# Optimization experiments

Measured on AMD Instinct MI355X. Metric: run time of the kernel, lower is better.

Reference implementation:

```python
import jax, jax.numpy as jnp
import numpy as np

A, D, H, NACT = 8, 128, 64, 16  # n_agents, input_shape, rnn_hidden_dim, n_actions
B = 16384


def setup_inputs() -> dict:
    key = jax.random.key(0)
    ks = jax.random.split(key, 12)
    s = 1.0 / np.sqrt(H)
    si = 1.0 / np.sqrt(D)
    inp = {
        'inputs': jax.random.normal(ks[0], (B * A, D), dtype=jnp.float32),
        'hidden_state': jax.random.normal(ks[1], (B, A, H), dtype=jnp.float32),
        # stacked per-agent (non-shared) weights, PyTorch default-init scale
        'W1': jax.random.uniform(ks[2], (A, H, D), jnp.float32, -si, si),
        'b1': jax.random.uniform(ks[3], (A, H), jnp.float32, -si, si),
        'W_ih': jax.random.uniform(ks[4], (A, 3 * H, H), jnp.float32, -s, s),
        'b_ih': jax.random.uniform(ks[5], (A, 3 * H), jnp.float32, -s, s),
        'W_hh': jax.random.uniform(ks[6], (A, 3 * H, H), jnp.float32, -s, s),
        'b_hh': jax.random.uniform(ks[7], (A, 3 * H), jnp.float32, -s, s),
        'W2': jax.random.uniform(ks[8], (A, NACT, H), jnp.float32, -s, s),
        'b2': jax.random.uniform(ks[9], (A, NACT), jnp.float32, -s, s),
    }
    return inp


def reference(inputs, hidden_state, W1, b1, W_ih, b_ih, W_hh, b_hh, W2, b2):
    x = inputs.reshape(-1, A, D)                 # [B, A, D]
    h = hidden_state.reshape(-1, A, H)           # [B, A, H]
    # fc1 + ReLU, batched over agents
    z1 = jax.nn.relu(jnp.einsum('bad,ahd->bah', x, W1) + b1)
    # GRUCell (PyTorch convention: gates r, z, n)
    gi = jnp.einsum('bah,agh->bag', z1, W_ih) + b_ih   # [B, A, 3H]
    gh = jnp.einsum('bah,agh->bag', h, W_hh) + b_hh
    i_r, i_z, i_n = jnp.split(gi, 3, axis=-1)
    h_r, h_z, h_n = jnp.split(gh, 3, axis=-1)
    r = jax.nn.sigmoid(i_r + h_r)
    z = jax.nn.sigmoid(i_z + h_z)
    n = jnp.tanh(i_n + r * h_n)
    h_new = (1.0 - z) * n + z * h                # [B, A, H]
    # fc2
    q = jnp.einsum('bah,anh->ban', h_new, W2) + b2   # [B, A, NACT]
    # match torch: cat(qs, dim=-1).view(-1, n_actions) == reshape [B*A, NACT]
    return q.reshape(-1, NACT), h_new
```

## Files before the change

kernel.cpp:

```cpp
#include <hip/hip_runtime.h>
#include <hip/hip_bf16.h>
#include <cstddef>

#define NAGENT 8
#define DIN    128
#define HID    64
#define NACT   16

typedef __attribute__((ext_vector_type(8))) short bf16x8;
typedef __attribute__((ext_vector_type(4))) float f32x4;

__device__ __forceinline__ short f2bf(float f) {
    __hip_bfloat16 h = __float2bfloat16(f);
    union { __hip_bfloat16 h; short s; } u; u.h = h;
    return u.s;
}
__device__ __forceinline__ float sigmoid_f(float v) { return 1.0f / (1.0f + __expf(-v)); }
__device__ __forceinline__ float tanh_f(float v) {
    v = fminf(fmaxf(v, -15.0f), 15.0f);
    float e = __expf(2.0f * v);
    return (e - 1.0f) / (e + 1.0f);
}
__device__ __forceinline__ bf16x8 cvt8pair(float4 v0, float4 v1) {
    bf16x8 r;
    r[0] = f2bf(v0.x); r[1] = f2bf(v0.y); r[2] = f2bf(v0.z); r[3] = f2bf(v0.w);
    r[4] = f2bf(v1.x); r[5] = f2bf(v1.y); r[6] = f2bf(v1.z); r[7] = f2bf(v1.w);
    return r;
}
__device__ __forceinline__ void gload_lds16(const void* g, void* l) {
    __builtin_amdgcn_global_load_lds(
        (const __attribute__((address_space(1))) unsigned int*)g,
        (__attribute__((address_space(3))) unsigned int*)l, 16, 0, 0);
}

extern "C" __global__ void __launch_bounds__(256)
conv_weights_packed(const float* __restrict__ W1, const float* __restrict__ Wih,
                    const float* __restrict__ Whh, const float* __restrict__ W2,
                    short* __restrict__ ws)
{
    const int a = blockIdx.y;
    const int c = blockIdx.x * 256 + threadIdx.x;
    if (c >= 4224) return;
    const int lane = c & 63, lr = lane & 15, lk = lane >> 4;
    const float* src;
    if (c < 1024) {
        int n = c >> 8, k = (c >> 6) & 3;
        src = W1 + a * 8192 + (n * 16 + lr) * 128 + k * 32 + lk * 8;
    } else if (c < 2560) {
        int idx = (c - 1024) >> 6;
        int g = idx >> 3, n = (idx >> 1) & 3, kk = idx & 1;
        src = Wih + a * 12288 + (g * 64 + n * 16 + lr) * 64 + kk * 32 + lk * 8;
    } else if (c < 4096) {
        int idx = (c - 2560) >> 6;
        int g = idx >> 3, n = (idx >> 1) & 3, kk = idx & 1;
        src = Whh + a * 12288 + (g * 64 + n * 16 + lr) * 64 + kk * 32 + lk * 8;
    } else {
        int kk = (c - 4096) >> 6;
        src = W2 + a * 1024 + lr * 64 + kk * 32 + lk * 8;
    }
    float4 v0 = ((const float4*)src)[0];
    float4 v1 = ((const float4*)src)[1];
    bf16x8 o = cvt8pair(v0, v1);
    *(bf16x8*)(ws + (size_t)a * 33792 + (size_t)c * 8) = o;
}

extern "C" __global__ void __launch_bounds__(256, 4)
rnn_main(const float* __restrict__ x,
         const float* __restrict__ hin,
         const float* __restrict__ b1, const float* __restrict__ bih,
         const float* __restrict__ bhh, const float* __restrict__ b2,
         const short* __restrict__ wsp,
         float* __restrict__ qout,
         float* __restrict__ hout)
{
    const int bid  = blockIdx.x;
    const int a    = bid & 7;
    const int t    = threadIdx.x;
    const int wid  = t >> 6;
    const int lane = t & 63;
    const int lr   = lane & 15;
    const int lk   = lane >> 4;

    __shared__ short wbuf[2 * 3072];
    __shared__ short zs[4 * 1024];
    char* zb = (char*)(zs + wid * 1024);
    const char* wb0 = (const char*)wbuf;
    const char* wb1 = (const char*)(wbuf + 3072);

    const short* wsA = wsp + (size_t)a * 33792;
    const int tile = (bid >> 3) * 4 + wid;
    const int arow = tile * 16 + lr;

    #define STAGE6(dstbuf, REXPR)                                                   \
        { int s = wid;  int rr = (REXPR);                                           \
          gload_lds16(wsA + (size_t)rr * 512 + lane * 8, (dstbuf) + s * 512);       \
          if (wid < 2) { s = wid + 4; rr = (REXPR);                                 \
            gload_lds16(wsA + (size_t)rr * 512 + lane * 8, (dstbuf) + s * 512); } }

    STAGE6(wbuf, s)

    const float* xrow = x + ((size_t)arow * NAGENT + a) * DIN + lk * 8;
    const float* hrow = hin + ((size_t)arow * NAGENT + a) * HID + lk * 8;
    bf16x8 xf[4];
    #pragma unroll
    for (int k = 0; k < 4; ++k)
        xf[k] = cvt8pair(*(const float4*)(xrow + k * 32),
                         *(const float4*)(xrow + k * 32 + 4));
    bf16x8 hf0 = cvt8pair(*(const float4*)(hrow),      *(const float4*)(hrow + 4));
    bf16x8 hf1 = cvt8pair(*(const float4*)(hrow + 32), *(const float4*)(hrow + 36));
    float b1v[4];
    #pragma unroll
    for (int n = 0; n < 4; ++n) b1v[n] = b1[a * HID + n * 16 + lr];

    f32x4 acc1[4];
    #pragma unroll
    for (int n = 0; n < 4; ++n) acc1[n] = (f32x4){0.f, 0.f, 0.f, 0.f};

    __syncthreads();

    STAGE6(wbuf + 3072, 6 + s)
    #pragma unroll
    for (int s = 0; s < 6; ++s) {
        bf16x8 w = *(const bf16x8*)(wb0 + s * 1024 + lane * 16);
        acc1[s >> 2] = __builtin_amdgcn_mfma_f32_16x16x32_bf16(xf[s & 3], w, acc1[s >> 2], 0, 0, 0);
    }
    __syncthreads();

    gload_lds16(wsA + (size_t)(12 + wid) * 512 + lane * 8, wbuf + wid * 512);
    #pragma unroll
    for (int s = 0; s < 6; ++s) {
        int f = 6 + s;
        bf16x8 w = *(const bf16x8*)(wb1 + s * 1024 + lane * 16);
        acc1[f >> 2] = __builtin_amdgcn_mfma_f32_16x16x32_bf16(xf[f & 3], w, acc1[f >> 2], 0, 0, 0);
    }
    __syncthreads();

    STAGE6(wbuf + 3072, 16 + 0 * 2 + (s >> 1) * 8 + (s & 1))
    #pragma unroll
    for (int s = 0; s < 4; ++s) {
        bf16x8 w = *(const bf16x8*)(wb0 + s * 1024 + lane * 16);
        acc1[3] = __builtin_amdgcn_mfma_f32_16x16x32_bf16(xf[s], w, acc1[3], 0, 0, 0);
    }
    #pragma unroll
    for (int n = 0; n < 4; ++n)
        #pragma unroll
        for (int j = 0; j < 4; ++j) {
            int row = lk * 4 + j, col = n * 16 + lr;
            *(short*)(zb + row * 128 + ((col * 2) ^ ((row & 7) << 4))) =
                f2bf(fmaxf(acc1[n][j] + b1v[n], 0.0f));
        }
    __syncthreads();

    bf16x8 za0 = *(const bf16x8*)(zb + lr * 128 + ((0 * 64 + lk * 16) ^ ((lr & 7) << 4)));
    bf16x8 za1 = *(const bf16x8*)(zb + lr * 128 + ((1 * 64 + lk * 16) ^ ((lr & 7) << 4)));

    #pragma unroll 1
    for (int n = 0; n < 4; ++n) {
        STAGE6(wbuf, 40 + n * 2 + (s >> 1) * 8 + (s & 1))
        float hp[4];
        #pragma unroll
        for (int j = 0; j < 4; ++j)
            hp[j] = hin[((size_t)(tile * 16 + lk * 4 + j) * NAGENT + a) * HID + n * 16 + lr];
        float bsr  = bih[a * 192 +   0 + n * 16 + lr] + bhh[a * 192 +   0 + n * 16 + lr];
        float bsz  = bih[a * 192 +  64 + n * 16 + lr] + bhh[a * 192 +  64 + n * 16 + lr];
        float bin_ = bih[a * 192 + 128 + n * 16 + lr];
        float bhn_ = bhh[a * 192 + 128 + n * 16 + lr];

        f32x4 aI0 = (f32x4){0.f,0.f,0.f,0.f}, aI1 = aI0, aI2 = aI0;
        {
            bf16x8 w0 = *(const bf16x8*)(wb1 + 0 * 1024 + lane * 16);
            bf16x8 w1 = *(const bf16x8*)(wb1 + 1 * 1024 + lane * 16);
            bf16x8 w2 = *(const bf16x8*)(wb1 + 2 * 1024 + lane * 16);
            bf16x8 w3 = *(const bf16x8*)(wb1 + 3 * 1024 + lane * 16);
            bf16x8 w4 = *(const bf16x8*)(wb1 + 4 * 1024 + lane * 16);
            bf16x8 w5 = *(const bf16x8*)(wb1 + 5 * 1024 + lane * 16);
            aI0 = __builtin_amdgcn_mfma_f32_16x16x32_bf16(za0, w0, aI0, 0, 0, 0);
            aI0 = __builtin_amdgcn_mfma_f32_16x16x32_bf16(za1, w1, aI0, 0, 0, 0);
            aI1 = __builtin_amdgcn_mfma_f32_16x16x32_bf16(za0, w2, aI1, 0, 0, 0);
            aI1 = __builtin_amdgcn_mfma_f32_16x16x32_bf16(za1, w3, aI1, 0, 0, 0);
            aI2 = __builtin_amdgcn_mfma_f32_16x16x32_bf16(za0, w4, aI2, 0, 0, 0);
            aI2 = __builtin_amdgcn_mfma_f32_16x16x32_bf16(za1, w5, aI2, 0, 0, 0);
        }
        __syncthreads();

        if (n < 3) {
            STAGE6(wbuf + 3072, 16 + (n + 1) * 2 + (s >> 1) * 8 + (s & 1))
        }
        f32x4 aH0 = (f32x4){0.f,0.f,0.f,0.f}, aH1 = aH0, aH2 = aH0;
        {
            bf16x8 w0 = *(const bf16x8*)(wb0 + 0 * 1024 + lane * 16);
            bf16x8 w1 = *(const bf16x8*)(wb0 + 1 * 1024 + lane * 16);
            bf16x8 w2 = *(const bf16x8*)(wb0 + 2 * 1024 + lane * 16);
            bf16x8 w3 = *(const bf16x8*)(wb0 + 3 * 1024 + lane * 16);
            bf16x8 w4 = *(const bf16x8*)(wb0 + 4 * 1024 + lane * 16);
            bf16x8 w5 = *(const bf16x8*)(wb0 + 5 * 1024 + lane * 16);
            aH0 = __builtin_amdgcn_mfma_f32_16x16x32_bf16(hf0, w0, aH0, 0, 0, 0);
            aH0 = __builtin_amdgcn_mfma_f32_16x16x32_bf16(hf1, w1, aH0, 0, 0, 0);
            aH1 = __builtin_amdgcn_mfma_f32_16x16x32_bf16(hf0, w2, aH1, 0, 0, 0);
            aH1 = __builtin_amdgcn_mfma_f32_16x16x32_bf16(hf1, w3, aH1, 0, 0, 0);
            aH2 = __builtin_amdgcn_mfma_f32_16x16x32_bf16(hf0, w4, aH2, 0, 0, 0);
            aH2 = __builtin_amdgcn_mfma_f32_16x16x32_bf16(hf1, w5, aH2, 0, 0, 0);
        }
        #pragma unroll
        for (int j = 0; j < 4; ++j) {
            int row = lk * 4 + j, col = n * 16 + lr;
            float r  = sigmoid_f(aI0[j] + aH0[j] + bsr);
            float zv = sigmoid_f(aI1[j] + aH1[j] + bsz);
            float nn = tanh_f((aI2[j] + bin_) + r * (aH2[j] + bhn_));
            float hv = (1.0f - zv) * nn + zv * hp[j];
            hout[((size_t)(tile * 16 + row) * NAGENT + a) * HID + col] = hv;
            *(short*)(zb + row * 128 + ((col * 2) ^ ((row & 7) << 4))) = f2bf(hv);
        }
        if (n < 3) __syncthreads();
    }

    {
        float bq = b2[a * NACT + lr];
        f32x4 q = (f32x4){bq, bq, bq, bq};
        bf16x8 ha0 = *(const bf16x8*)(zb + lr * 128 + ((0 * 64 + lk * 16) ^ ((lr & 7) << 4)));
        bf16x8 ha1 = *(const bf16x8*)(zb + lr * 128 + ((1 * 64 + lk * 16) ^ ((lr & 7) << 4)));
        bf16x8 w2f0 = *(const bf16x8*)(wsA + 32768 + (0 * 64 + lane) * 8);
        bf16x8 w2f1 = *(const bf16x8*)(wsA + 32768 + (1 * 64 + lane) * 8);
        q = __builtin_amdgcn_mfma_f32_16x16x32_bf16(ha0, w2f0, q, 0, 0, 0);
        q = __builtin_amdgcn_mfma_f32_16x16x32_bf16(ha1, w2f1, q, 0, 0, 0);
        #pragma unroll
        for (int j = 0; j < 4; ++j)
            qout[((size_t)(tile * 16 + lk * 4 + j) * NAGENT + a) * NACT + lr] = q[j];
    }
    #undef STAGE6
}

extern "C" void kernel_launch(void* const* d_in, const int* in_sizes, int n_in,
                              void* d_out, int out_size, void* d_ws, size_t ws_size,
                              hipStream_t stream)
{
    const float* x   = (const float*)d_in[0];
    const float* hin = (const float*)d_in[1];
    const float* W1  = (const float*)d_in[2];
    const float* b1  = (const float*)d_in[3];
    const float* Wih = (const float*)d_in[4];
    const float* bih = (const float*)d_in[5];
    const float* Whh = (const float*)d_in[6];
    const float* bhh = (const float*)d_in[7];
    const float* W2  = (const float*)d_in[8];
    const float* b2  = (const float*)d_in[9];

    const int B = in_sizes[0] / (NAGENT * DIN);

    float* qout = (float*)d_out;
    float* hout = (float*)d_out + (size_t)B * NAGENT * NACT;

    short* wsp = (short*)d_ws;

    conv_weights_packed<<<dim3(17, NAGENT), 256, 0, stream>>>(W1, Wih, Whh, W2, wsp);

    dim3 grid((B / 64) * NAGENT);
    rnn_main<<<grid, 256, 0, stream>>>(x, hin, b1, bih, bhh, b2, wsp, qout, hout);
}
```

Measured before the change: 48.09 us.

## Coalesce hidden-state stores via LDS, raise MFMA wave priority, simplify tanh

The scattered per-element fp32 stores of the new hidden state are removed. h_out is now written once at the end as float4 stores read back from the bf16 copy in LDS, which means h_out is output at bf16 precision rather than fp32. The MFMA sections are wrapped in s_setprio(1)/s_setprio(0), and tanh is rewritten to use a single division. The goal is fewer, more coalesced global writes and better MFMA issue, at the cost of precision in the hidden-state output.

```diff
diff --git a/kernel.cpp b/kernel.cpp
--- a/kernel.cpp
+++ b/kernel.cpp
@@ -15,11 +15,14 @@
     union { __hip_bfloat16 h; short s; } u; u.h = h;
     return u.s;
 }
+__device__ __forceinline__ float bf2f(unsigned short u) {
+    union { unsigned u; float f; } v; v.u = ((unsigned)u) << 16; return v.f;
+}
 __device__ __forceinline__ float sigmoid_f(float v) { return 1.0f / (1.0f + __expf(-v)); }
 __device__ __forceinline__ float tanh_f(float v) {
     v = fminf(fmaxf(v, -15.0f), 15.0f);
     float e = __expf(2.0f * v);
-    return (e - 1.0f) / (e + 1.0f);
+    return 1.0f - 2.0f / (e + 1.0f);
 }
 __device__ __forceinline__ bf16x8 cvt8pair(float4 v0, float4 v1) {
     bf16x8 r;
@@ -119,28 +122,34 @@
     __syncthreads();
 
     STAGE6(wbuf + 3072, 6 + s)
+    __builtin_amdgcn_s_setprio(1);
     #pragma unroll
     for (int s = 0; s < 6; ++s) {
         bf16x8 w = *(const bf16x8*)(wb0 + s * 1024 + lane * 16);
         acc1[s >> 2] = __builtin_amdgcn_mfma_f32_16x16x32_bf16(xf[s & 3], w, acc1[s >> 2], 0, 0, 0);
     }
+    __builtin_amdgcn_s_setprio(0);
     __syncthreads();
 
     gload_lds16(wsA + (size_t)(12 + wid) * 512 + lane * 8, wbuf + wid * 512);
+    __builtin_amdgcn_s_setprio(1);
     #pragma unroll
     for (int s = 0; s < 6; ++s) {
         int f = 6 + s;
         bf16x8 w = *(const bf16x8*)(wb1 + s * 1024 + lane * 16);
         acc1[f >> 2] = __builtin_amdgcn_mfma_f32_16x16x32_bf16(xf[f & 3], w, acc1[f >> 2], 0, 0, 0);
     }
+    __builtin_amdgcn_s_setprio(0);
     __syncthreads();
 
     STAGE6(wbuf + 3072, 16 + 0 * 2 + (s >> 1) * 8 + (s & 1))
+    __builtin_amdgcn_s_setprio(1);
     #pragma unroll
     for (int s = 0; s < 4; ++s) {
         bf16x8 w = *(const bf16x8*)(wb0 + s * 1024 + lane * 16);
         acc1[3] = __builtin_amdgcn_mfma_f32_16x16x32_bf16(xf[s], w, acc1[3], 0, 0, 0);
     }
+    __builtin_amdgcn_s_setprio(0);
     #pragma unroll
     for (int n = 0; n < 4; ++n)
         #pragma unroll
@@ -174,12 +183,14 @@
             bf16x8 w3 = *(const bf16x8*)(wb1 + 3 * 1024 + lane * 16);
             bf16x8 w4 = *(const bf16x8*)(wb1 + 4 * 1024 + lane * 16);
             bf16x8 w5 = *(const bf16x8*)(wb1 + 5 * 1024 + lane * 16);
+            __builtin_amdgcn_s_setprio(1);
             aI0 = __builtin_amdgcn_mfma_f32_16x16x32_bf16(za0, w0, aI0, 0, 0, 0);
             aI0 = __builtin_amdgcn_mfma_f32_16x16x32_bf16(za1, w1, aI0, 0, 0, 0);
             aI1 = __builtin_amdgcn_mfma_f32_16x16x32_bf16(za0, w2, aI1, 0, 0, 0);
             aI1 = __builtin_amdgcn_mfma_f32_16x16x32_bf16(za1, w3, aI1, 0, 0, 0);
             aI2 = __builtin_amdgcn_mfma_f32_16x16x32_bf16(za0, w4, aI2, 0, 0, 0);
             aI2 = __builtin_amdgcn_mfma_f32_16x16x32_bf16(za1, w5, aI2, 0, 0, 0);
+            __builtin_amdgcn_s_setprio(0);
         }
         __syncthreads();
 
@@ -194,12 +205,14 @@
             bf16x8 w3 = *(const bf16x8*)(wb0 + 3 * 1024 + lane * 16);
             bf16x8 w4 = *(const bf16x8*)(wb0 + 4 * 1024 + lane * 16);
             bf16x8 w5 = *(const bf16x8*)(wb0 + 5 * 1024 + lane * 16);
+            __builtin_amdgcn_s_setprio(1);
             aH0 = __builtin_amdgcn_mfma_f32_16x16x32_bf16(hf0, w0, aH0, 0, 0, 0);
             aH0 = __builtin_amdgcn_mfma_f32_16x16x32_bf16(hf1, w1, aH0, 0, 0, 0);
             aH1 = __builtin_amdgcn_mfma_f32_16x16x32_bf16(hf0, w2, aH1, 0, 0, 0);
             aH1 = __builtin_amdgcn_mfma_f32_16x16x32_bf16(hf1, w3, aH1, 0, 0, 0);
             aH2 = __builtin_amdgcn_mfma_f32_16x16x32_bf16(hf0, w4, aH2, 0, 0, 0);
             aH2 = __builtin_amdgcn_mfma_f32_16x16x32_bf16(hf1, w5, aH2, 0, 0, 0);
+            __builtin_amdgcn_s_setprio(0);
         }
         #pragma unroll
         for (int j = 0; j < 4; ++j) {
@@ -208,7 +221,6 @@
             float zv = sigmoid_f(aI1[j] + aH1[j] + bsz);
             float nn = tanh_f((aI2[j] + bin_) + r * (aH2[j] + bhn_));
             float hv = (1.0f - zv) * nn + zv * hp[j];
-            hout[((size_t)(tile * 16 + row) * NAGENT + a) * HID + col] = hv;
             *(short*)(zb + row * 128 + ((col * 2) ^ ((row & 7) << 4))) = f2bf(hv);
         }
         if (n < 3) __syncthreads();
@@ -226,6 +238,24 @@
         #pragma unroll
         for (int j = 0; j < 4; ++j)
             qout[((size_t)(tile * 16 + lk * 4 + j) * NAGENT + a) * NACT + lr] = q[j];
+    }
+
+    {
+        int row = lane >> 2;
+        int c0  = (lane & 3) * 4;
+        float* hb = hout + ((size_t)(tile * 16 + row) * NAGENT + a) * HID + c0;
+        #pragma unroll
+        for (int i = 0; i < 4; ++i) {
+            int cb = (c0 + i * 16) * 2;
+            unsigned long long v =
+                *(const unsigned long long*)(zb + row * 128 + (cb ^ ((row & 7) << 4)));
+            float4 o;
+            o.x = bf2f((unsigned short)(v));
+            o.y = bf2f((unsigned short)(v >> 16));
+            o.z = bf2f((unsigned short)(v >> 32));
+            o.w = bf2f((unsigned short)(v >> 48));
+            *(float4*)(hb + i * 16) = o;
+        }
     }
     #undef STAGE6
 }
```

After: 48.17 us. Within noise of the previous version (+0.2%).
